# Kernel tuning notes

Hardware: AMD Instinct MI355X
Metric: run time of the kernel (lower is better)

## Reference

```python
import jax, jax.numpy as jnp
import numpy as np

N = 2048
FEAT = 64

def setup_inputs() -> dict:
    key = jax.random.key(0)
    ks = jax.random.split(key, 9)
    s = lambda fan_in: 1.0 / np.sqrt(fan_in)
    return {
        "asset_features": jax.random.normal(ks[0], (N, FEAT), jnp.float32),
        "Wp": jax.random.uniform(ks[1], (32, FEAT), jnp.float32, -s(FEAT), s(FEAT)),
        "bp": jax.random.uniform(ks[2], (32,), jnp.float32, -s(FEAT), s(FEAT)),
        "W1": jax.random.uniform(ks[3], (32, 64), jnp.float32, -s(64), s(64)),
        "b1": jax.random.uniform(ks[4], (32,), jnp.float32, -s(64), s(64)),
        "W2": jax.random.uniform(ks[5], (16, 32), jnp.float32, -s(32), s(32)),
        "b2": jax.random.uniform(ks[6], (16,), jnp.float32, -s(32), s(32)),
        "W3": jax.random.uniform(ks[7], (1, 16), jnp.float32, -s(16), s(16)),
        "b3": jax.random.uniform(ks[8], (1,), jnp.float32, -s(16), s(16)),
    }

def reference(asset_features, Wp, bp, W1, b1, W2, b2, W3, b3):
    n = asset_features.shape[0]
    # projected: [N, 32]
    proj = asset_features @ Wp.T + bp
    # First similarity layer acts on concat([proj_i, proj_j]) of size 64.
    # Split W1 into the halves acting on i-features and j-features so we
    # never materialize the [N, N, 64] concat tensor.
    Wa, Wb = W1[:, :32], W1[:, 32:]
    pa = proj @ Wa.T            # [N, 32] contribution of row asset i
    pb = proj @ Wb.T            # [N, 32] contribution of col asset j
    h1 = jax.nn.relu(pa[:, None, :] + pb[None, :, :] + b1)   # [N, N, 32]
    h2 = jax.nn.relu(jnp.einsum('ijk,hk->ijh', h1, W2) + b2)  # [N, N, 16]
    sim = jax.nn.sigmoid(jnp.einsum('ijh,h->ij', h2, W3[0]) + b3[0])  # [N, N]
    # Diagonal forced to 1.0, matching fill_diagonal_(1.0)
    eye = jnp.eye(n, dtype=bool)
    return jnp.where(eye, jnp.float32(1.0), sim)
```

## Files before the change

kernel.cpp:

```cpp
#include <hip/hip_runtime.h>
#include <hip/hip_fp16.h>

#define NN 2048

typedef _Float16 f16x8 __attribute__((ext_vector_type(8)));
typedef float f32x16 __attribute__((ext_vector_type(16)));

__global__ __launch_bounds__(256) void prep_kernel(
    const float* __restrict__ A, const float* __restrict__ Wp,
    const float* __restrict__ bp, const float* __restrict__ W1,
    const float* __restrict__ b1,
    _Float16* __restrict__ pa, _Float16* __restrict__ pb)
{
    __shared__ float projLDS[8][32];
    const int t = threadIdx.x;
    const int rl = t >> 5;
    const int k  = t & 31;
    const int row = blockIdx.x * 8 + rl;

    const float4* xa = (const float4*)(A + row * 64);
    const float4* wp = (const float4*)(Wp + k * 64);
    float acc = bp[k];
#pragma unroll
    for (int m = 0; m < 16; ++m) {
        float4 xv = xa[m], wv = wp[m];
        acc += xv.x * wv.x + xv.y * wv.y + xv.z * wv.z + xv.w * wv.w;
    }
    projLDS[rl][k] = acc;
    __syncthreads();

    const float4* w1a = (const float4*)(W1 + k * 64);
    const float4* w1b = (const float4*)(W1 + k * 64 + 32);
    const float4* pr  = (const float4*)(projLDS[rl]);
    float sa = b1[k], sb = 0.f;
#pragma unroll
    for (int m = 0; m < 8; ++m) {
        float4 p = pr[m], wa = w1a[m], wb = w1b[m];
        sa += p.x * wa.x + p.y * wa.y + p.z * wa.z + p.w * wa.w;
        sb += p.x * wb.x + p.y * wb.y + p.z * wb.z + p.w * wb.w;
    }
    pa[row * 32 + k] = (_Float16)sa;
    pb[row * 32 + k] = (_Float16)sb;
}

__global__ __launch_bounds__(256) void sim_kernel(
    const _Float16* __restrict__ pa, const _Float16* __restrict__ pb,
    const float* __restrict__ W2, const float* __restrict__ b2,
    const float* __restrict__ W3, const float* __restrict__ b3,
    float* __restrict__ out)
{
    __shared__ _Float16 paLDS[32 * 32];
    const int t    = threadIdx.x;
    const int lane = t & 63;
    const int wid  = t >> 6;
    const int i0 = (blockIdx.x >> 4) * 32;
    const int jb = (((blockIdx.x & 15) << 2) + wid) * 32;
    const int p  = lane & 31;
    const int g  = lane >> 5;

    ((uint2*)paLDS)[t] = ((const uint2*)(pa + (size_t)i0 * 32))[t];

    const _Float16* pbrow = pb + (size_t)(jb + p) * 32;
    f16x8 pblo = *(const f16x8*)(pbrow + g * 8);
    f16x8 pbhi = *(const f16x8*)(pbrow + 16 + g * 8);

    f16x8 w2lo = {};
    f16x8 w2hi = {};
    if (p < 16) {
        const float* w2r = W2 + p * 32;
#pragma unroll
        for (int e = 0; e < 8; ++e) {
            w2lo[e] = (_Float16)w2r[g * 8 + e];
            w2hi[e] = (_Float16)w2r[16 + g * 8 + e];
        }
    }

    float w3r[8];
    f32x16 cinit;
#pragma unroll
    for (int r = 0; r < 4; ++r) {
        w3r[r]       = W3[4 * g + r];
        w3r[4 + r]   = W3[8 + 4 * g + r];
        cinit[r]     = b2[4 * g + r];
        cinit[4 + r] = b2[8 + 4 * g + r];
    }
#pragma unroll
    for (int r = 8; r < 16; ++r) cinit[r] = 0.f;

    const float b3v = b3[0];
    const f16x8 zero = {};
    const int j = jb + p;

    __syncthreads();

#pragma unroll 4
    for (int ii = 0; ii < 32; ++ii) {
        const int i = i0 + ii;
        f16x8 alo = *(const f16x8*)&paLDS[ii * 32 + g * 8];
        f16x8 ahi = *(const f16x8*)&paLDS[ii * 32 + 16 + g * 8];
        f16x8 h1lo = __builtin_elementwise_max(alo + pblo, zero);
        f16x8 h1hi = __builtin_elementwise_max(ahi + pbhi, zero);

        f32x16 d = __builtin_amdgcn_mfma_f32_32x32x16_f16(w2lo, h1lo, cinit, 0, 0, 0);
        d        = __builtin_amdgcn_mfma_f32_32x32x16_f16(w2hi, h1hi, d,     0, 0, 0);

        float partial = 0.f;
#pragma unroll
        for (int r = 0; r < 8; ++r)
            partial = fmaf(fmaxf(d[r], 0.f), w3r[r], partial);
        partial += __shfl_xor(partial, 32, 64);
        const float z = partial + b3v;
        float sim = __builtin_amdgcn_rcpf(1.f + __expf(-z));
        if (i == j) sim = 1.f;
        if (lane < 32) out[(size_t)i * NN + j] = sim;
    }
}

extern "C" void kernel_launch(void* const* d_in, const int* in_sizes, int n_in,
                              void* d_out, int out_size, void* d_ws, size_t ws_size,
                              hipStream_t stream)
{
    const float* A  = (const float*)d_in[0];
    const float* Wp = (const float*)d_in[1];
    const float* bp = (const float*)d_in[2];
    const float* W1 = (const float*)d_in[3];
    const float* b1 = (const float*)d_in[4];
    const float* W2 = (const float*)d_in[5];
    const float* b2 = (const float*)d_in[6];
    const float* W3 = (const float*)d_in[7];
    const float* b3 = (const float*)d_in[8];
    float* out = (float*)d_out;

    _Float16* pa = (_Float16*)d_ws;
    _Float16* pb = pa + NN * 32;

    prep_kernel<<<NN / 8, 256, 0, stream>>>(A, Wp, bp, W1, b1, pa, pb);
    sim_kernel<<<1024, 256, 0, stream>>>(pa, pb, W2, b2, W3, b3, out);
}
```

Baseline: 99.00 us.

## Process two rows per iteration, use all lanes for sigmoid and store, double grid

Each block now covers 16 rows instead of 32, and the grid doubles to 2048 blocks with a launch-bounds occupancy hint. Each loop iteration handles two rows with interleaved independent MFMA chains. The two half-wavefronts then split the sigmoid and store work, so all 64 lanes write useful output instead of only half. The aim is better MFMA latency hiding, no wasted lanes in the epilogue, and more blocks to fill the GPU, at the cost of more per-block setup (W2 conversion, pb loads) relative to useful work.

Measured after the change: 93.78 us. 1.06x faster.

```diff
diff --git a/kernel.cpp b/kernel.cpp
--- a/kernel.cpp
+++ b/kernel.cpp
@@ -43,22 +43,22 @@
     pb[row * 32 + k] = (_Float16)sb;
 }
 
-__global__ __launch_bounds__(256) void sim_kernel(
+__global__ __launch_bounds__(256, 4) void sim_kernel(
     const _Float16* __restrict__ pa, const _Float16* __restrict__ pb,
     const float* __restrict__ W2, const float* __restrict__ b2,
     const float* __restrict__ W3, const float* __restrict__ b3,
     float* __restrict__ out)
 {
-    __shared__ _Float16 paLDS[32 * 32];
+    __shared__ _Float16 paLDS[16 * 32];
     const int t    = threadIdx.x;
     const int lane = t & 63;
     const int wid  = t >> 6;
-    const int i0 = (blockIdx.x >> 4) * 32;
+    const int i0 = (blockIdx.x >> 4) * 16;
     const int jb = (((blockIdx.x & 15) << 2) + wid) * 32;
     const int p  = lane & 31;
     const int g  = lane >> 5;
 
-    ((uint2*)paLDS)[t] = ((const uint2*)(pa + (size_t)i0 * 32))[t];
+    ((uint*)paLDS)[t] = ((const uint*)(pa + (size_t)i0 * 32))[t];
 
     const _Float16* pbrow = pb + (size_t)(jb + p) * 32;
     f16x8 pblo = *(const f16x8*)(pbrow + g * 8);
@@ -89,30 +89,43 @@
 
     const float b3v = b3[0];
     const f16x8 zero = {};
-    const int j = jb + p;
+    const int jlane = jb + p;
+    float* outp = out + (size_t)g * NN + jlane;
 
     __syncthreads();
 
-#pragma unroll 4
-    for (int ii = 0; ii < 32; ++ii) {
-        const int i = i0 + ii;
-        f16x8 alo = *(const f16x8*)&paLDS[ii * 32 + g * 8];
-        f16x8 ahi = *(const f16x8*)&paLDS[ii * 32 + 16 + g * 8];
-        f16x8 h1lo = __builtin_elementwise_max(alo + pblo, zero);
-        f16x8 h1hi = __builtin_elementwise_max(ahi + pbhi, zero);
+#pragma unroll 2
+    for (int tt = 0; tt < 8; ++tt) {
+        const int iA = i0 + 2 * tt;
+        const _Float16* rowA = &paLDS[(2 * tt) * 32];
+        const _Float16* rowB = &paLDS[(2 * tt + 1) * 32];
+        f16x8 aAlo = *(const f16x8*)(rowA + g * 8);
+        f16x8 aAhi = *(const f16x8*)(rowA + 16 + g * 8);
+        f16x8 aBlo = *(const f16x8*)(rowB + g * 8);
+        f16x8 aBhi = *(const f16x8*)(rowB + 16 + g * 8);
+        f16x8 hAlo = __builtin_elementwise_max(aAlo + pblo, zero);
+        f16x8 hAhi = __builtin_elementwise_max(aAhi + pbhi, zero);
+        f16x8 hBlo = __builtin_elementwise_max(aBlo + pblo, zero);
+        f16x8 hBhi = __builtin_elementwise_max(aBhi + pbhi, zero);
 
-        f32x16 d = __builtin_amdgcn_mfma_f32_32x32x16_f16(w2lo, h1lo, cinit, 0, 0, 0);
-        d        = __builtin_amdgcn_mfma_f32_32x32x16_f16(w2hi, h1hi, d,     0, 0, 0);
+        f32x16 dA = __builtin_amdgcn_mfma_f32_32x32x16_f16(w2lo, hAlo, cinit, 0, 0, 0);
+        f32x16 dB = __builtin_amdgcn_mfma_f32_32x32x16_f16(w2lo, hBlo, cinit, 0, 0, 0);
+        dA        = __builtin_amdgcn_mfma_f32_32x32x16_f16(w2hi, hAhi, dA,    0, 0, 0);
+        dB        = __builtin_amdgcn_mfma_f32_32x32x16_f16(w2hi, hBhi, dB,    0, 0, 0);
 
-        float partial = 0.f;
+        float pA = 0.f, pB = 0.f;
 #pragma unroll
-        for (int r = 0; r < 8; ++r)
-            partial = fmaf(fmaxf(d[r], 0.f), w3r[r], partial);
-        partial += __shfl_xor(partial, 32, 64);
-        const float z = partial + b3v;
+        for (int r = 0; r < 8; ++r) {
+            pA = fmaf(fmaxf(dA[r], 0.f), w3r[r], pA);
+            pB = fmaf(fmaxf(dB[r], 0.f), w3r[r], pB);
+        }
+        pA += __shfl_xor(pA, 32, 64);
+        pB += __shfl_xor(pB, 32, 64);
+
+        const float z = (g == 0 ? pA : pB) + b3v;
         float sim = __builtin_amdgcn_rcpf(1.f + __expf(-z));
-        if (i == j) sim = 1.f;
-        if (lane < 32) out[(size_t)i * NN + j] = sim;
+        if (iA + g == jlane) sim = 1.f;
+        outp[(size_t)iA * NN] = sim;
     }
 }
 
@@ -135,5 +148,5 @@
     _Float16* pb = pa + NN * 32;
 
     prep_kernel<<<NN / 8, 256, 0, stream>>>(A, Wp, bp, W1, b1, pa, pb);
-    sim_kernel<<<1024, 256, 0, stream>>>(pa, pb, W2, b2, W3, b3, out);
+    sim_kernel<<<2048, 256, 0, stream>>>(pa, pb, W2, b2, W3, b3, out);
 }
```

## Switch sim kernel to 16x16x32 MFMA without padded W2 rows

Applied to the files above, without the earlier changes.

Replaces the pair of 32x32x16 MFMAs, where half of the M rows were zero padding for the 16-output W2 layer, with a single 16x16x32 MFMA per (i, 16-column tile). Each wave now covers 16 columns, and all 64 lanes store results by spreading four i rows across lane quarters, so no lanes sit idle on writes. The grid doubles and the launch bounds ask for higher occupancy. In exchange there are more shuffles per output and narrower 64-byte store segments per row.

Result: faster. 94.31 us (-4.7%).

```diff
diff --git a/kernel.cpp b/kernel.cpp
--- a/kernel.cpp
+++ b/kernel.cpp
@@ -4,7 +4,7 @@
 #define NN 2048
 
 typedef _Float16 f16x8 __attribute__((ext_vector_type(8)));
-typedef float f32x16 __attribute__((ext_vector_type(16)));
+typedef float f32x4 __attribute__((ext_vector_type(4)));
 
 __global__ __launch_bounds__(256) void prep_kernel(
     const float* __restrict__ A, const float* __restrict__ Wp,
@@ -43,7 +43,7 @@
     pb[row * 32 + k] = (_Float16)sb;
 }
 
-__global__ __launch_bounds__(256) void sim_kernel(
+__global__ __launch_bounds__(256, 8) void sim_kernel(
     const _Float16* __restrict__ pa, const _Float16* __restrict__ pb,
     const float* __restrict__ W2, const float* __restrict__ b2,
     const float* __restrict__ W3, const float* __restrict__ b3,
@@ -53,66 +53,59 @@
     const int t    = threadIdx.x;
     const int lane = t & 63;
     const int wid  = t >> 6;
-    const int i0 = (blockIdx.x >> 4) * 32;
-    const int jb = (((blockIdx.x & 15) << 2) + wid) * 32;
-    const int p  = lane & 31;
-    const int g  = lane >> 5;
+    const int i0 = (blockIdx.x >> 5) * 32;
+    const int jb = (((blockIdx.x & 31) << 2) + wid) * 16;
+    const int n  = lane & 15;
+    const int q  = lane >> 4;
 
     ((uint2*)paLDS)[t] = ((const uint2*)(pa + (size_t)i0 * 32))[t];
 
-    const _Float16* pbrow = pb + (size_t)(jb + p) * 32;
-    f16x8 pblo = *(const f16x8*)(pbrow + g * 8);
-    f16x8 pbhi = *(const f16x8*)(pbrow + 16 + g * 8);
+    const f16x8 pbf = *(const f16x8*)(pb + (size_t)(jb + n) * 32 + q * 8);
 
-    f16x8 w2lo = {};
-    f16x8 w2hi = {};
-    if (p < 16) {
-        const float* w2r = W2 + p * 32;
+    f16x8 w2f;
+    {
+        const float* w2r = W2 + n * 32 + q * 8;
 #pragma unroll
-        for (int e = 0; e < 8; ++e) {
-            w2lo[e] = (_Float16)w2r[g * 8 + e];
-            w2hi[e] = (_Float16)w2r[16 + g * 8 + e];
-        }
+        for (int e = 0; e < 8; ++e) w2f[e] = (_Float16)w2r[e];
     }
 
-    float w3r[8];
-    f32x16 cinit;
+    f32x4 cinit;
+    float w3r[4];
 #pragma unroll
     for (int r = 0; r < 4; ++r) {
-        w3r[r]       = W3[4 * g + r];
-        w3r[4 + r]   = W3[8 + 4 * g + r];
-        cinit[r]     = b2[4 * g + r];
-        cinit[4 + r] = b2[8 + 4 * g + r];
+        cinit[r] = b2[q * 4 + r];
+        w3r[r]   = W3[q * 4 + r];
     }
-#pragma unroll
-    for (int r = 8; r < 16; ++r) cinit[r] = 0.f;
-
     const float b3v = b3[0];
     const f16x8 zero = {};
-    const int j = jb + p;
 
     __syncthreads();
 
-#pragma unroll 4
-    for (int ii = 0; ii < 32; ++ii) {
-        const int i = i0 + ii;
-        f16x8 alo = *(const f16x8*)&paLDS[ii * 32 + g * 8];
-        f16x8 ahi = *(const f16x8*)&paLDS[ii * 32 + 16 + g * 8];
-        f16x8 h1lo = __builtin_elementwise_max(alo + pblo, zero);
-        f16x8 h1hi = __builtin_elementwise_max(ahi + pbhi, zero);
+    float* outp = out + (size_t)(i0 + q) * NN + jb + n;
 
-        f32x16 d = __builtin_amdgcn_mfma_f32_32x32x16_f16(w2lo, h1lo, cinit, 0, 0, 0);
-        d        = __builtin_amdgcn_mfma_f32_32x32x16_f16(w2hi, h1hi, d,     0, 0, 0);
-
-        float partial = 0.f;
+#pragma unroll 2
+    for (int tt = 0; tt < 8; ++tt) {
+        float s0, s1, s2, s3;
 #pragma unroll
-        for (int r = 0; r < 8; ++r)
-            partial = fmaf(fmaxf(d[r], 0.f), w3r[r], partial);
-        partial += __shfl_xor(partial, 32, 64);
-        const float z = partial + b3v;
+        for (int r4 = 0; r4 < 4; ++r4) {
+            const int ii = 4 * tt + r4;
+            f16x8 af = *(const f16x8*)&paLDS[ii * 32 + q * 8];
+            f16x8 h1 = __builtin_elementwise_max(af + pbf, zero);
+            f32x4 d = __builtin_amdgcn_mfma_f32_16x16x32_f16(w2f, h1, cinit, 0, 0, 0);
+            float p = 0.f;
+#pragma unroll
+            for (int r = 0; r < 4; ++r)
+                p = fmaf(fmaxf(d[r], 0.f), w3r[r], p);
+            p += __shfl_xor(p, 16, 64);
+            p += __shfl_xor(p, 32, 64);
+            if (r4 == 0) s0 = p; else if (r4 == 1) s1 = p;
+            else if (r4 == 2) s2 = p; else s3 = p;
+        }
+        const float z = (q < 2 ? (q == 0 ? s0 : s1) : (q == 2 ? s2 : s3)) + b3v;
         float sim = __builtin_amdgcn_rcpf(1.f + __expf(-z));
-        if (i == j) sim = 1.f;
-        if (lane < 32) out[(size_t)i * NN + j] = sim;
+        const int iMine = i0 + 4 * tt + q;
+        if (iMine == jb + n) sim = 1.f;
+        outp[(size_t)(4 * tt) * NN] = sim;
     }
 }
 
@@ -135,5 +128,5 @@
     _Float16* pb = pa + NN * 32;
 
     prep_kernel<<<NN / 8, 256, 0, stream>>>(A, Wp, bp, W1, b1, pa, pb);
-    sim_kernel<<<1024, 256, 0, stream>>>(pa, pb, W2, b2, W3, b3, out);
+    sim_kernel<<<2048, 256, 0, stream>>>(pa, pb, W2, b2, W3, b3, out);
 }
```
